# Optimization experiments

Measured on AMD Instinct MI355X. Metric: run time of the kernel, lower is better.

The kernel has to match this reference:

```python
import jax, jax.numpy as jnp
import numpy as np

B, S, E = 8, 1024, 1024
H, DH = 16, 64          # num_head, num_hidden (per-head dim); H*DH == E
DFF, K = 2048, 3        # d_ff hardcoded in EncoderBlock; kernel_size
LN_EPS = 1e-5


def _layer_norm(x):
    # Fresh torch.nn.LayerNorm each call -> gamma=1, beta=0
    mu = jnp.mean(x, axis=-1, keepdims=True)
    var = jnp.mean((x - mu) ** 2, axis=-1, keepdims=True)
    return (x - mu) / jnp.sqrt(var + LN_EPS)


def _causal_conv1d(x, w, b, k):
    # x: [B, C_in, S], w: [C_out, C_in, k] (torch Conv1d layout), left-pad k-1 -> causal
    y = jax.lax.conv_general_dilated(
        x, w, window_strides=(1,), padding=[(k - 1, 0)],
        dimension_numbers=("NCH", "OIH", "NCH"))
    return y + b[None, :, None]


def setup_inputs() -> dict:
    key = jax.random.key(0)
    ks = jax.random.split(key, 14)
    sc = 0.02
    inp = {
        "word": jax.random.normal(ks[0], (B, S, E), jnp.float32),
        # torch Linear weights: [out, in]
        "Wq": jax.random.normal(ks[1], (H * DH, E), jnp.float32) * sc,
        "bq": jnp.zeros((H * DH,), jnp.float32),
        "Wk": jax.random.normal(ks[2], (H * DH, E), jnp.float32) * sc,
        "bk": jnp.zeros((H * DH,), jnp.float32),
        "Wv": jax.random.normal(ks[3], (H * DH, E), jnp.float32) * sc,
        "bv": jnp.zeros((H * DH,), jnp.float32),
        "Wo": jax.random.normal(ks[4], (E, H * DH), jnp.float32) * sc,
        "bo": jnp.zeros((E,), jnp.float32),
        # torch Conv1d weights: [out_ch, in_ch, k]
        "conv1_w": jax.random.normal(ks[5], (DFF, E, K), jnp.float32) * sc,
        "conv1_b": jnp.zeros((DFF,), jnp.float32),
        "conv2_w": jax.random.normal(ks[6], (E, DFF, K), jnp.float32) * sc,
        "conv2_b": jnp.zeros((E,), jnp.float32),
    }
    return inp


def reference(word, Wq, bq, Wk, bk, Wv, bv, Wo, bo, conv1_w, conv1_b, conv2_w, conv2_b):
    # ---- Multi-head self-attention (isMasked=False), dropout = identity (eval) ----
    q = (word @ Wq.T + bq).reshape(B, S, H, DH)   # [B,S,H,DH]
    k = (word @ Wk.T + bk).reshape(B, S, H, DH)
    v = (word @ Wv.T + bv).reshape(B, S, H, DH)
    scores = jnp.einsum("bihd,bjhd->bhij", q, k) / np.sqrt(DH)  # [B,H,S,S]
    attn = jax.nn.softmax(scores, axis=-1)
    outs = jnp.einsum("bhij,bjhd->bihd", attn, v).reshape(B, S, H * DH)
    outs = outs @ Wo.T + bo
    x = _layer_norm(outs + word)                  # residual + LayerNorm

    # ---- Causal conv FFN (k>1 branch) ----
    x_ = jnp.swapaxes(x, -1, -2)                  # [B,E,S]
    h = jax.nn.relu(_causal_conv1d(x_, conv1_w, conv1_b, K))  # [B,DFF,S]
    y = _causal_conv1d(h, conv2_w, conv2_b, K)    # [B,E,S]
    y = jnp.swapaxes(y, -1, -2)                   # [B,S,E]
    out = _layer_norm(y + x)
    return out, attn
```

## Files before the change

kernel.cpp:

```cpp
#include <hip/hip_runtime.h>
#include <stdint.h>

#define B_ 8
#define S_ 1024
#define E_ 1024
#define H_ 16
#define DH_ 64
#define DFF_ 2048
#define KCONV 3

typedef unsigned short u16;
typedef __attribute__((ext_vector_type(8))) short short8;
typedef __attribute__((ext_vector_type(4))) float floatx4;
typedef __attribute__((ext_vector_type(4))) unsigned int uintx4;

__device__ __forceinline__ u16 f2bf(float f) {
  unsigned int u = __builtin_bit_cast(unsigned int, f);
  u += 0x7FFFu + ((u >> 16) & 1u);
  return (u16)(u >> 16);
}
__device__ __forceinline__ float bf2f(u16 x) {
  unsigned int u = ((unsigned int)x) << 16;
  return __builtin_bit_cast(float, u);
}

__device__ __forceinline__ uintx4 ld8_f32_bf(const float* __restrict__ p) {
  floatx4 a = *(const floatx4*)p;
  floatx4 b = *(const floatx4*)(p + 4);
  uintx4 r;
  r.x = (unsigned)f2bf(a[0]) | ((unsigned)f2bf(a[1]) << 16);
  r.y = (unsigned)f2bf(a[2]) | ((unsigned)f2bf(a[3]) << 16);
  r.z = (unsigned)f2bf(b[0]) | ((unsigned)f2bf(b[1]) << 16);
  r.w = (unsigned)f2bf(b[2]) | ((unsigned)f2bf(b[3]) << 16);
  return r;
}

__device__ __forceinline__ void gload16(const void* g, void* l) {
  __builtin_amdgcn_global_load_lds((__attribute__((address_space(1))) void*)g,
                                   (__attribute__((address_space(3))) void*)l,
                                   16, 0, 0);
}

enum { F_BIAS = 1, F_RELU = 2, F_RESID = 4, F_OUTF32 = 8, F_SCALE = 16 };

template <int WR, int WC, int TAPS, int FLAGS, bool AF32, bool WF32>
__global__ void __launch_bounds__(256, 2)
gemm_kernel(const void* __restrict__ A, long aS1, long aS2,
            const void* __restrict__ W, long wS1, long wS2,
            const float* __restrict__ bias, const float* __restrict__ resid,
            void* __restrict__ Cout, long cS1, long cS2,
            int zdiv, int lda, int ldw, int ldc, int Kin, float scale) {
  constexpr bool GL = !AF32 && !WF32;
  constexpr int BM = WR * 64, BN = WC * 64, BK = 64;
  constexpr int LDP = GL ? BK : BK + 8;
  __shared__ __align__(16) u16 As[BM * LDP];
  __shared__ __align__(16) u16 Bs[BN * LDP];

  const int z = blockIdx.z;
  const int zq = z / zdiv, zr = z % zdiv;
  const u16* Ab16 = (const u16*)A + zq * aS1 + zr * aS2;
  const float* Ab32 = (const float*)A + zq * aS1 + zr * aS2;
  const u16* Wb16 = (const u16*)W + zq * wS1 + zr * wS2;
  const float* Wb32 = (const float*)W + zq * wS1 + zr * wS2;
  const long cOff = zq * cS1 + zr * cS2;

  const int m0 = blockIdx.y * BM;
  const int n0 = blockIdx.x * BN;
  const int tid = threadIdx.x;
  const int lane = tid & 63;
  const int wave = tid >> 6;
  const int wrow = wave / WC;
  const int wcol = wave % WC;
  const int lm = lane & 15;
  const int lk = lane >> 4;

  floatx4 acc[4][4];
#pragma unroll
  for (int r = 0; r < 4; ++r)
#pragma unroll
    for (int c = 0; c < 4; ++c) acc[r][c] = floatx4{0.f, 0.f, 0.f, 0.f};

  for (int t = 0; t < TAPS; ++t) {
    for (int k0 = 0; k0 < Kin; k0 += BK) {
      __syncthreads();
      if constexpr (GL) {
#pragma unroll
        for (int it = 0; it < BM * BK / 8 / 256; ++it) {
          int c = tid + it * 256;
          int row = c >> 3;
          int kc = (c & 7) << 3;
          long arow = m0 + row;
          if (TAPS > 1) arow += t - (TAPS - 1);
          gload16(Ab16 + arow * (long)lda + k0 + kc,
                  (char*)As + it * 4096 + wave * 1024);
        }
#pragma unroll
        for (int it = 0; it < BN * BK / 8 / 256; ++it) {
          int c = tid + it * 256;
          int row = c >> 3;
          int kc = (c & 7) << 3;
          long off = (long)(n0 + row) * ldw + (long)t * Kin + k0 + kc;
          gload16(Wb16 + off, (char*)Bs + it * 4096 + wave * 1024);
        }
      } else {
#pragma unroll
        for (int it = 0; it < BM * BK / 8 / 256; ++it) {
          int c = tid + it * 256;
          int row = c >> 3;
          int kc = (c & 7) << 3;
          int grow = m0 + row;
          long arow = grow;
          bool zero = false;
          if (TAPS > 1) {
            int s = grow & (S_ - 1);
            if (s + t - (TAPS - 1) < 0) zero = true;
            arow = (long)grow + t - (TAPS - 1);
          }
          uintx4 val;
          if (zero)
            val = uintx4{0u, 0u, 0u, 0u};
          else if (AF32)
            val = ld8_f32_bf(Ab32 + arow * lda + k0 + kc);
          else
            val = *(const uintx4*)(Ab16 + arow * lda + k0 + kc);
          *(uintx4*)&As[row * LDP + kc] = val;
        }
#pragma unroll
        for (int it = 0; it < BN * BK / 8 / 256; ++it) {
          int c = tid + it * 256;
          int row = c >> 3;
          int kc = (c & 7) << 3;
          long off = (long)(n0 + row) * ldw + (long)t * Kin + k0 + kc;
          uintx4 val;
          if (WF32)
            val = ld8_f32_bf(Wb32 + off);
          else
            val = *(const uintx4*)(Wb16 + off);
          *(uintx4*)&Bs[row * LDP + kc] = val;
        }
      }
      __syncthreads();
      if constexpr (GL && TAPS > 1) {
        if ((m0 & (S_ - 1)) == 0 && t < TAPS - 1) {
          int nz = TAPS - 1 - t;
          if (tid < nz * 8) {
            int row = tid >> 3;
            int kc = (tid & 7) << 3;
            *(uintx4*)&As[row * LDP + kc] = uintx4{0u, 0u, 0u, 0u};
          }
          __syncthreads();
        }
      }
#pragma unroll
      for (int kk = 0; kk < BK; kk += 32) {
        short8 af[4], bfr[4];
#pragma unroll
        for (int r = 0; r < 4; ++r)
          af[r] = *(const short8*)&As[(wrow * 64 + r * 16 + lm) * LDP + kk + lk * 8];
#pragma unroll
        for (int c = 0; c < 4; ++c)
          bfr[c] = *(const short8*)&Bs[(wcol * 64 + c * 16 + lm) * LDP + kk + lk * 8];
#pragma unroll
        for (int r = 0; r < 4; ++r)
#pragma unroll
          for (int c = 0; c < 4; ++c)
            acc[r][c] = __builtin_amdgcn_mfma_f32_16x16x32_bf16(af[r], bfr[c], acc[r][c], 0, 0, 0);
      }
    }
  }

  float* Cf = (float*)Cout;
  u16* Cb = (u16*)Cout;
#pragma unroll
  for (int r = 0; r < 4; ++r) {
#pragma unroll
    for (int c = 0; c < 4; ++c) {
#pragma unroll
      for (int i = 0; i < 4; ++i) {
        int grow = m0 + wrow * 64 + r * 16 + lk * 4 + i;
        int gcol = n0 + wcol * 64 + c * 16 + lm;
        float v = acc[r][c][i];
        if (FLAGS & F_SCALE) v *= scale;
        if (FLAGS & F_BIAS) v += bias[gcol];
        long off = cOff + (long)grow * ldc + gcol;
        if (FLAGS & F_RESID) v += resid[off];
        if (FLAGS & F_RELU) v = v > 0.f ? v : 0.f;
        if (FLAGS & F_OUTF32)
          Cf[off] = v;
        else
          Cb[off] = f2bf(v);
      }
    }
  }
}

__global__ void __launch_bounds__(256)
convert_bf16(const float* __restrict__ in, u16* __restrict__ out, long n) {
  long i = ((long)blockIdx.x * 256 + threadIdx.x) * 8;
  if (i >= n) return;
  *(uintx4*)(out + i) = ld8_f32_bf(in + i);
}

__global__ void __launch_bounds__(256)
softmax_kernel(float* __restrict__ attn) {
  long row = blockIdx.x;
  float* p = attn + row * (long)S_;
  int tid = threadIdx.x;
  float v[4];
  float mx = -3.4e38f;
#pragma unroll
  for (int i = 0; i < 4; ++i) {
    v[i] = p[tid + i * 256];
    mx = fmaxf(mx, v[i]);
  }
#pragma unroll
  for (int o = 32; o > 0; o >>= 1) mx = fmaxf(mx, __shfl_down(mx, o));
  __shared__ float sm[4];
  __shared__ float ss[4];
  if ((tid & 63) == 0) sm[tid >> 6] = mx;
  __syncthreads();
  mx = fmaxf(fmaxf(sm[0], sm[1]), fmaxf(sm[2], sm[3]));
  float s = 0.f;
#pragma unroll
  for (int i = 0; i < 4; ++i) {
    v[i] = __expf(v[i] - mx);
    s += v[i];
  }
#pragma unroll
  for (int o = 32; o > 0; o >>= 1) s += __shfl_down(s, o);
  if ((tid & 63) == 0) ss[tid >> 6] = s;
  __syncthreads();
  s = ss[0] + ss[1] + ss[2] + ss[3];
  float inv = 1.f / s;
#pragma unroll
  for (int i = 0; i < 4; ++i) p[tid + i * 256] = v[i] * inv;
}

template <bool ADD2, bool STOREBF, bool STOREF32>
__global__ void __launch_bounds__(256)
ln_kernel(const float* __restrict__ in1, const float* __restrict__ in2,
          u16* __restrict__ outb, float* __restrict__ outf) {
  long row = blockIdx.x;
  const float* p1 = in1 + row * E_;
  int tid = threadIdx.x;
  float v[4];
  float s = 0.f, s2 = 0.f;
#pragma unroll
  for (int i = 0; i < 4; ++i) {
    float x = p1[tid + i * 256];
    if (ADD2) x += in2[row * E_ + tid + i * 256];
    v[i] = x;
    s += x;
    s2 += x * x;
  }
#pragma unroll
  for (int o = 32; o > 0; o >>= 1) {
    s += __shfl_down(s, o);
    s2 += __shfl_down(s2, o);
  }
  __shared__ float as_[4];
  __shared__ float bs_[4];
  if ((tid & 63) == 0) {
    as_[tid >> 6] = s;
    bs_[tid >> 6] = s2;
  }
  __syncthreads();
  s = as_[0] + as_[1] + as_[2] + as_[3];
  s2 = bs_[0] + bs_[1] + bs_[2] + bs_[3];
  float mean = s * (1.f / E_);
  float var = s2 * (1.f / E_) - mean * mean;
  float rstd = rsqrtf(var + 1e-5f);
#pragma unroll
  for (int i = 0; i < 4; ++i) {
    float y = (v[i] - mean) * rstd;
    if (STOREBF) outb[row * E_ + tid + i * 256] = f2bf(y);
    if (STOREF32) outf[row * E_ + tid + i * 256] = y;
  }
}

__global__ void __launch_bounds__(256)
transpose_v(const u16* __restrict__ v, u16* __restrict__ vT) {
  int bh = blockIdx.y;
  int b = bh / H_, h = bh % H_;
  int s0 = blockIdx.x * 64;
  __shared__ u16 t[64][65];
  int tid = threadIdx.x;
#pragma unroll
  for (int i = 0; i < 16; ++i) {
    int idx = tid + i * 256;
    int r = idx >> 6, c = idx & 63;
    t[r][c] = v[(long)b * S_ * E_ + (long)(s0 + r) * E_ + h * DH_ + c];
  }
  __syncthreads();
#pragma unroll
  for (int i = 0; i < 16; ++i) {
    int idx = tid + i * 256;
    int d = idx >> 6, c = idx & 63;
    vT[((long)bh * DH_ + d) * S_ + s0 + c] = t[c][d];
  }
}

__global__ void __launch_bounds__(256)
transpose_w(const float* __restrict__ w, u16* __restrict__ wt, int F, int Cin) {
  long n = (long)F * Cin * KCONV;
  long i = (long)blockIdx.x * 256 + threadIdx.x;
  if (i >= n) return;
  int e = (int)(i % Cin);
  long tmp = i / Cin;
  int t = (int)(tmp % KCONV);
  int f = (int)(tmp / KCONV);
  wt[i] = f2bf(w[(long)f * Cin * KCONV + (long)e * KCONV + t]);
}

extern "C" void kernel_launch(void* const* d_in, const int* in_sizes, int n_in,
                              void* d_out, int out_size, void* d_ws, size_t ws_size,
                              hipStream_t stream) {
  const float* word = (const float*)d_in[0];
  const float* Wq = (const float*)d_in[1];
  const float* bq = (const float*)d_in[2];
  const float* Wk = (const float*)d_in[3];
  const float* bk = (const float*)d_in[4];
  const float* Wv = (const float*)d_in[5];
  const float* bv = (const float*)d_in[6];
  const float* Wo = (const float*)d_in[7];
  const float* bo = (const float*)d_in[8];
  const float* w1 = (const float*)d_in[9];
  const float* b1 = (const float*)d_in[10];
  const float* w2 = (const float*)d_in[11];
  const float* b2 = (const float*)d_in[12];

  const long MB = 1048576L;
  char* ws = (char*)d_ws;
  u16* q_bf = (u16*)(ws + 0 * MB);
  u16* k_bf = (u16*)(ws + 16 * MB);
  u16* v_bf = (u16*)(ws + 32 * MB);
  u16* vT = (u16*)(ws + 48 * MB);
  u16* outs_bf = (u16*)(ws + 64 * MB);
  u16* w1t = (u16*)(ws + 80 * MB);
  u16* w2t = (u16*)(ws + 92 * MB);
  float* z_f32 = (float*)(ws + 0 * MB);
  u16* x_bf = (u16*)(ws + 32 * MB);
  float* x_f32 = (float*)(ws + 104 * MB);
  u16* h_bf = (u16*)(ws + 136 * MB);
  float* y_f32 = (float*)(ws + 48 * MB);
  u16* word_bf = (u16*)(ws + 104 * MB);
  u16* wq_bf = (u16*)(ws + 136 * MB);
  u16* wk_bf = (u16*)(ws + 138 * MB);
  u16* wv_bf = (u16*)(ws + 140 * MB);
  u16* wo_bf = (u16*)(ws + 142 * MB);

  float* out_f = (float*)d_out;
  float* attn_f = (float*)d_out + (long)B_ * S_ * E_;

  dim3 blk(256);

  {
    long n1 = (long)DFF_ * E_ * KCONV;
    transpose_w<<<dim3((unsigned)((n1 + 255) / 256)), blk, 0, stream>>>(w1, w1t, DFF_, E_);
    long n2 = (long)E_ * DFF_ * KCONV;
    transpose_w<<<dim3((unsigned)((n2 + 255) / 256)), blk, 0, stream>>>(w2, w2t, E_, DFF_);
  }
  {
    long nw = (long)B_ * S_ * E_;
    convert_bf16<<<dim3((unsigned)(nw / 8 / 256)), blk, 0, stream>>>(word, word_bf, nw);
    long nl = (long)E_ * E_;
    unsigned gl = (unsigned)(nl / 8 / 256);
    convert_bf16<<<dim3(gl), blk, 0, stream>>>(Wq, wq_bf, nl);
    convert_bf16<<<dim3(gl), blk, 0, stream>>>(Wk, wk_bf, nl);
    convert_bf16<<<dim3(gl), blk, 0, stream>>>(Wv, wv_bf, nl);
    convert_bf16<<<dim3(gl), blk, 0, stream>>>(Wo, wo_bf, nl);
  }

  dim3 g_sq(E_ / 128, (B_ * S_) / 128, 1);
  gemm_kernel<2, 2, 1, F_BIAS, false, false><<<g_sq, blk, 0, stream>>>(
      word_bf, 0, 0, wq_bf, 0, 0, bq, nullptr, q_bf, 0, 0, 1, E_, E_, E_, E_, 1.f);
  gemm_kernel<2, 2, 1, F_BIAS, false, false><<<g_sq, blk, 0, stream>>>(
      word_bf, 0, 0, wk_bf, 0, 0, bk, nullptr, k_bf, 0, 0, 1, E_, E_, E_, E_, 1.f);
  gemm_kernel<2, 2, 1, F_BIAS, false, false><<<g_sq, blk, 0, stream>>>(
      word_bf, 0, 0, wv_bf, 0, 0, bv, nullptr, v_bf, 0, 0, 1, E_, E_, E_, E_, 1.f);

  dim3 g_sc(S_ / 128, S_ / 128, B_ * H_);
  gemm_kernel<2, 2, 1, F_SCALE | F_OUTF32, false, false><<<g_sc, blk, 0, stream>>>(
      q_bf, (long)S_ * E_, DH_, k_bf, (long)S_ * E_, DH_, nullptr, nullptr,
      attn_f, (long)H_ * S_ * S_, (long)S_ * S_, H_, E_, E_, S_, DH_, 0.125f);

  softmax_kernel<<<dim3(B_ * H_ * S_), blk, 0, stream>>>(attn_f);

  transpose_v<<<dim3(S_ / 64, B_ * H_), blk, 0, stream>>>(v_bf, vT);

  dim3 g_av(1, S_ / 256, B_ * H_);
  gemm_kernel<4, 1, 1, 0, true, false><<<g_av, blk, 0, stream>>>(
      attn_f, (long)H_ * S_ * S_, (long)S_ * S_, vT, (long)H_ * DH_ * S_, (long)DH_ * S_,
      nullptr, nullptr, outs_bf, (long)S_ * E_, DH_, H_, S_, S_, E_, S_, 1.f);

  gemm_kernel<2, 2, 1, F_BIAS | F_RESID | F_OUTF32, false, false><<<g_sq, blk, 0, stream>>>(
      outs_bf, 0, 0, wo_bf, 0, 0, bo, word, z_f32, 0, 0, 1, E_, E_, E_, E_, 1.f);

  ln_kernel<false, true, true><<<dim3(B_ * S_), blk, 0, stream>>>(z_f32, nullptr, x_bf, x_f32);

  dim3 g_c1(DFF_ / 128, (B_ * S_) / 128, 1);
  gemm_kernel<2, 2, 3, F_BIAS | F_RELU, false, false><<<g_c1, blk, 0, stream>>>(
      x_bf, 0, 0, w1t, 0, 0, b1, nullptr, h_bf, 0, 0, 1, E_, KCONV * E_, DFF_, E_, 1.f);

  dim3 g_c2(E_ / 128, (B_ * S_) / 128, 1);
  gemm_kernel<2, 2, 3, F_BIAS | F_OUTF32, false, false><<<g_c2, blk, 0, stream>>>(
      h_bf, 0, 0, w2t, 0, 0, b2, nullptr, y_f32, 0, 0, 1, DFF_, KCONV * DFF_, E_, DFF_, 1.f);

  ln_kernel<true, false, true><<<dim3(B_ * S_), blk, 0, stream>>>(y_f32, x_f32, nullptr, out_f);
}
```

Measured before the change: 1.531 ms.

## Store raw scores in bf16 and recompute softmax inside the PV GEMM load

The QK^T GEMM now writes raw scaled scores as bf16 into a workspace buffer instead of fp32 into the attention output. A finalize kernel computes per-row max and inverse sum, writes the fp32 attn output once, and saves the stats. The PV GEMM then reads the bf16 raw scores and applies exp/normalize on the fly, so it no longer reads the fp32 attn matrix and the in-place fp32 read-modify-write softmax pass goes away. This needs a large workspace and falls back to the old path otherwise; it adds redundant exp work in the GEMM loader, and softmax on bf16-rounded scores may lose accuracy.

```diff
diff --git a/kernel.cpp b/kernel.cpp
--- a/kernel.cpp
+++ b/kernel.cpp
@@ -13,6 +13,7 @@
 typedef __attribute__((ext_vector_type(8))) short short8;
 typedef __attribute__((ext_vector_type(4))) float floatx4;
 typedef __attribute__((ext_vector_type(4))) unsigned int uintx4;
+typedef __attribute__((ext_vector_type(2))) unsigned int uintx2;
 
 __device__ __forceinline__ u16 f2bf(float f) {
   unsigned int u = __builtin_bit_cast(unsigned int, f);
@@ -41,20 +42,31 @@
                                    16, 0, 0);
 }
 
+__device__ __forceinline__ unsigned softpair(unsigned w, float m, float invl) {
+  float a = bf2f((u16)(w & 0xffffu));
+  float b = bf2f((u16)(w >> 16));
+  a = __expf(a - m) * invl;
+  b = __expf(b - m) * invl;
+  return (unsigned)f2bf(a) | ((unsigned)f2bf(b) << 16);
+}
+
 enum { F_BIAS = 1, F_RELU = 2, F_RESID = 4, F_OUTF32 = 8, F_SCALE = 16 };
 
-template <int WR, int WC, int TAPS, int FLAGS, bool AF32, bool WF32>
+template <int WR, int WC, int TAPS, int FLAGS, bool AF32, bool WF32, bool ASOFT>
 __global__ void __launch_bounds__(256, 2)
 gemm_kernel(const void* __restrict__ A, long aS1, long aS2,
             const void* __restrict__ W, long wS1, long wS2,
             const float* __restrict__ bias, const float* __restrict__ resid,
+            const float2* __restrict__ astats,
             void* __restrict__ Cout, long cS1, long cS2,
             int zdiv, int lda, int ldw, int ldc, int Kin, float scale) {
-  constexpr bool GL = !AF32 && !WF32;
+  constexpr bool GLA = !AF32 && !ASOFT;
+  constexpr bool GLB = !WF32;
   constexpr int BM = WR * 64, BN = WC * 64, BK = 64;
-  constexpr int LDP = GL ? BK : BK + 8;
-  __shared__ __align__(16) u16 As[BM * LDP];
-  __shared__ __align__(16) u16 Bs[BN * LDP];
+  constexpr int LDPA = GLA ? BK : BK + 8;
+  constexpr int LDPB = GLB ? BK : BK + 8;
+  __shared__ __align__(16) u16 As[BM * LDPA];
+  __shared__ __align__(16) u16 Bs[BN * LDPB];
 
   const int z = blockIdx.z;
   const int zq = z / zdiv, zr = z % zdiv;
@@ -83,7 +95,7 @@
   for (int t = 0; t < TAPS; ++t) {
     for (int k0 = 0; k0 < Kin; k0 += BK) {
       __syncthreads();
-      if constexpr (GL) {
+      if constexpr (GLA) {
 #pragma unroll
         for (int it = 0; it < BM * BK / 8 / 256; ++it) {
           int c = tid + it * 256;
@@ -93,14 +105,6 @@
           if (TAPS > 1) arow += t - (TAPS - 1);
           gload16(Ab16 + arow * (long)lda + k0 + kc,
                   (char*)As + it * 4096 + wave * 1024);
-        }
-#pragma unroll
-        for (int it = 0; it < BN * BK / 8 / 256; ++it) {
-          int c = tid + it * 256;
-          int row = c >> 3;
-          int kc = (c & 7) << 3;
-          long off = (long)(n0 + row) * ldw + (long)t * Kin + k0 + kc;
-          gload16(Wb16 + off, (char*)Bs + it * 4096 + wave * 1024);
         }
       } else {
 #pragma unroll
@@ -119,12 +123,30 @@
           uintx4 val;
           if (zero)
             val = uintx4{0u, 0u, 0u, 0u};
-          else if (AF32)
+          else if (ASOFT) {
+            uintx4 raw = *(const uintx4*)(Ab16 + arow * lda + k0 + kc);
+            float2 st = astats[(long)z * S_ + grow];
+            val.x = softpair(raw.x, st.x, st.y);
+            val.y = softpair(raw.y, st.x, st.y);
+            val.z = softpair(raw.z, st.x, st.y);
+            val.w = softpair(raw.w, st.x, st.y);
+          } else if (AF32)
             val = ld8_f32_bf(Ab32 + arow * lda + k0 + kc);
           else
             val = *(const uintx4*)(Ab16 + arow * lda + k0 + kc);
-          *(uintx4*)&As[row * LDP + kc] = val;
+          *(uintx4*)&As[row * LDPA + kc] = val;
         }
+      }
+      if constexpr (GLB) {
+#pragma unroll
+        for (int it = 0; it < BN * BK / 8 / 256; ++it) {
+          int c = tid + it * 256;
+          int row = c >> 3;
+          int kc = (c & 7) << 3;
+          long off = (long)(n0 + row) * ldw + (long)t * Kin + k0 + kc;
+          gload16(Wb16 + off, (char*)Bs + it * 4096 + wave * 1024);
+        }
+      } else {
 #pragma unroll
         for (int it = 0; it < BN * BK / 8 / 256; ++it) {
           int c = tid + it * 256;
@@ -136,17 +158,17 @@
             val = ld8_f32_bf(Wb32 + off);
           else
             val = *(const uintx4*)(Wb16 + off);
-          *(uintx4*)&Bs[row * LDP + kc] = val;
+          *(uintx4*)&Bs[row * LDPB + kc] = val;
         }
       }
       __syncthreads();
-      if constexpr (GL && TAPS > 1) {
+      if constexpr (GLA && TAPS > 1) {
         if ((m0 & (S_ - 1)) == 0 && t < TAPS - 1) {
           int nz = TAPS - 1 - t;
           if (tid < nz * 8) {
             int row = tid >> 3;
             int kc = (tid & 7) << 3;
-            *(uintx4*)&As[row * LDP + kc] = uintx4{0u, 0u, 0u, 0u};
+            *(uintx4*)&As[row * LDPA + kc] = uintx4{0u, 0u, 0u, 0u};
           }
           __syncthreads();
         }
@@ -156,10 +178,10 @@
         short8 af[4], bfr[4];
 #pragma unroll
         for (int r = 0; r < 4; ++r)
-          af[r] = *(const short8*)&As[(wrow * 64 + r * 16 + lm) * LDP + kk + lk * 8];
+          af[r] = *(const short8*)&As[(wrow * 64 + r * 16 + lm) * LDPA + kk + lk * 8];
 #pragma unroll
         for (int c = 0; c < 4; ++c)
-          bfr[c] = *(const short8*)&Bs[(wcol * 64 + c * 16 + lm) * LDP + kk + lk * 8];
+          bfr[c] = *(const short8*)&Bs[(wcol * 64 + c * 16 + lm) * LDPB + kk + lk * 8];
 #pragma unroll
         for (int r = 0; r < 4; ++r)
 #pragma unroll
@@ -234,6 +256,45 @@
   float inv = 1.f / s;
 #pragma unroll
   for (int i = 0; i < 4; ++i) p[tid + i * 256] = v[i] * inv;
+}
+
+__global__ void __launch_bounds__(256)
+softmax_finalize(const u16* __restrict__ raw, float* __restrict__ attn,
+                 float2* __restrict__ stats) {
+  long row = blockIdx.x;
+  const u16* p = raw + row * (long)S_;
+  int tid = threadIdx.x;
+  uintx2 w = *(const uintx2*)(p + tid * 4);
+  float v[4];
+  v[0] = bf2f((u16)(w.x & 0xffffu));
+  v[1] = bf2f((u16)(w.x >> 16));
+  v[2] = bf2f((u16)(w.y & 0xffffu));
+  v[3] = bf2f((u16)(w.y >> 16));
+  float mx = fmaxf(fmaxf(v[0], v[1]), fmaxf(v[2], v[3]));
+#pragma unroll
+  for (int o = 32; o > 0; o >>= 1) mx = fmaxf(mx, __shfl_down(mx, o));
+  __shared__ float sm[4];
+  __shared__ float ss[4];
+  if ((tid & 63) == 0) sm[tid >> 6] = mx;
+  __syncthreads();
+  mx = fmaxf(fmaxf(sm[0], sm[1]), fmaxf(sm[2], sm[3]));
+  float s = 0.f;
+#pragma unroll
+  for (int i = 0; i < 4; ++i) {
+    v[i] = __expf(v[i] - mx);
+    s += v[i];
+  }
+#pragma unroll
+  for (int o = 32; o > 0; o >>= 1) s += __shfl_down(s, o);
+  if ((tid & 63) == 0) ss[tid >> 6] = s;
+  __syncthreads();
+  s = ss[0] + ss[1] + ss[2] + ss[3];
+  float inv = 1.f / s;
+  floatx4 outv;
+#pragma unroll
+  for (int i = 0; i < 4; ++i) outv[i] = v[i] * inv;
+  *(floatx4*)(attn + row * (long)S_ + tid * 4) = outv;
+  if (tid == 0) stats[row] = make_float2(mx, inv);
 }
 
 template <bool ADD2, bool STOREBF, bool STOREF32>
@@ -348,6 +409,9 @@
   u16* wk_bf = (u16*)(ws + 138 * MB);
   u16* wv_bf = (u16*)(ws + 140 * MB);
   u16* wo_bf = (u16*)(ws + 142 * MB);
+  u16* raw_bf = (u16*)(ws + 144 * MB);
+  float2* stats = (float2*)(ws + 400 * MB);
+  const bool big_ws = ws_size >= (size_t)(402 * MB);
 
   float* out_f = (float*)d_out;
   float* attn_f = (float*)d_out + (long)B_ * S_ * E_;
@@ -372,39 +436,50 @@
   }
 
   dim3 g_sq(E_ / 128, (B_ * S_) / 128, 1);
-  gemm_kernel<2, 2, 1, F_BIAS, false, false><<<g_sq, blk, 0, stream>>>(
-      word_bf, 0, 0, wq_bf, 0, 0, bq, nullptr, q_bf, 0, 0, 1, E_, E_, E_, E_, 1.f);
-  gemm_kernel<2, 2, 1, F_BIAS, false, false><<<g_sq, blk, 0, stream>>>(
-      word_bf, 0, 0, wk_bf, 0, 0, bk, nullptr, k_bf, 0, 0, 1, E_, E_, E_, E_, 1.f);
-  gemm_kernel<2, 2, 1, F_BIAS, false, false><<<g_sq, blk, 0, stream>>>(
-      word_bf, 0, 0, wv_bf, 0, 0, bv, nullptr, v_bf, 0, 0, 1, E_, E_, E_, E_, 1.f);
+  gemm_kernel<2, 2, 1, F_BIAS, false, false, false><<<g_sq, blk, 0, stream>>>(
+      word_bf, 0, 0, wq_bf, 0, 0, bq, nullptr, nullptr, q_bf, 0, 0, 1, E_, E_, E_, E_, 1.f);
+  gemm_kernel<2, 2, 1, F_BIAS, false, false, false><<<g_sq, blk, 0, stream>>>(
+      word_bf, 0, 0, wk_bf, 0, 0, bk, nullptr, nullptr, k_bf, 0, 0, 1, E_, E_, E_, E_, 1.f);
+  gemm_kernel<2, 2, 1, F_BIAS, false, false, false><<<g_sq, blk, 0, stream>>>(
+      word_bf, 0, 0, wv_bf, 0, 0, bv, nullptr, nullptr, v_bf, 0, 0, 1, E_, E_, E_, E_, 1.f);
 
   dim3 g_sc(S_ / 128, S_ / 128, B_ * H_);
-  gemm_kernel<2, 2, 1, F_SCALE | F_OUTF32, false, false><<<g_sc, blk, 0, stream>>>(
-      q_bf, (long)S_ * E_, DH_, k_bf, (long)S_ * E_, DH_, nullptr, nullptr,
-      attn_f, (long)H_ * S_ * S_, (long)S_ * S_, H_, E_, E_, S_, DH_, 0.125f);
-
-  softmax_kernel<<<dim3(B_ * H_ * S_), blk, 0, stream>>>(attn_f);
+  dim3 g_av(1, S_ / 256, B_ * H_);
 
   transpose_v<<<dim3(S_ / 64, B_ * H_), blk, 0, stream>>>(v_bf, vT);
 
-  dim3 g_av(1, S_ / 256, B_ * H_);
-  gemm_kernel<4, 1, 1, 0, true, false><<<g_av, blk, 0, stream>>>(
-      attn_f, (long)H_ * S_ * S_, (long)S_ * S_, vT, (long)H_ * DH_ * S_, (long)DH_ * S_,
-      nullptr, nullptr, outs_bf, (long)S_ * E_, DH_, H_, S_, S_, E_, S_, 1.f);
-
-  gemm_kernel<2, 2, 1, F_BIAS | F_RESID | F_OUTF32, false, false><<<g_sq, blk, 0, stream>>>(
-      outs_bf, 0, 0, wo_bf, 0, 0, bo, word, z_f32, 0, 0, 1, E_, E_, E_, E_, 1.f);
+  if (big_ws) {
+    gemm_kernel<2, 2, 1, F_SCALE, false, false, false><<<g_sc, blk, 0, stream>>>(
+        q_bf, (long)S_ * E_, DH_, k_bf, (long)S_ * E_, DH_, nullptr, nullptr, nullptr,
+        raw_bf, (long)H_ * S_ * S_, (long)S_ * S_, H_, E_, E_, S_, DH_, 0.125f);
+
+    softmax_finalize<<<dim3(B_ * H_ * S_), blk, 0, stream>>>(raw_bf, attn_f, stats);
+
+    gemm_kernel<4, 1, 1, 0, false, false, true><<<g_av, blk, 0, stream>>>(
+        raw_bf, (long)H_ * S_ * S_, (long)S_ * S_, vT, (long)H_ * DH_ * S_, (long)DH_ * S_,
+        nullptr, nullptr, stats, outs_bf, (long)S_ * E_, DH_, H_, S_, S_, E_, S_, 1.f);
+  } else {
+    gemm_kernel<2, 2, 1, F_SCALE | F_OUTF32, false, false, false><<<g_sc, blk, 0, stream>>>(
+        q_bf, (long)S_ * E_, DH_, k_bf, (long)S_ * E_, DH_, nullptr, nullptr, nullptr,
+        attn_f, (long)H_ * S_ * S_, (long)S_ * S_, H_, E_, E_, S_, DH_, 0.125f);
+    softmax_kernel<<<dim3(B_ * H_ * S_), blk, 0, stream>>>(attn_f);
+    gemm_kernel<4, 1, 1, 0, true, false, false><<<g_av, blk, 0, stream>>>(
+        attn_f, (long)H_ * S_ * S_, (long)S_ * S_, vT, (long)H_ * DH_ * S_, (long)DH_ * S_,
+        nullptr, nullptr, nullptr, outs_bf, (long)S_ * E_, DH_, H_, S_, S_, E_, S_, 1.f);
+  }
+
+  gemm_kernel<2, 2, 1, F_BIAS | F_RESID | F_OUTF32, false, false, false><<<g_sq, blk, 0, stream>>>(
+      outs_bf, 0, 0, wo_bf, 0, 0, bo, word, nullptr, z_f32, 0, 0, 1, E_, E_, E_, E_, 1.f);
 
   ln_kernel<false, true, true><<<dim3(B_ * S_), blk, 0, stream>>>(z_f32, nullptr, x_bf, x_f32);
 
   dim3 g_c1(DFF_ / 128, (B_ * S_) / 128, 1);
-  gemm_kernel<2, 2, 3, F_BIAS | F_RELU, false, false><<<g_c1, blk, 0, stream>>>(
-      x_bf, 0, 0, w1t, 0, 0, b1, nullptr, h_bf, 0, 0, 1, E_, KCONV * E_, DFF_, E_, 1.f);
+  gemm_kernel<2, 2, 3, F_BIAS | F_RELU, false, false, false><<<g_c1, blk, 0, stream>>>(
+      x_bf, 0, 0, w1t, 0, 0, b1, nullptr, nullptr, h_bf, 0, 0, 1, E_, KCONV * E_, DFF_, E_, 1.f);
 
   dim3 g_c2(E_ / 128, (B_ * S_) / 128, 1);
-  gemm_kernel<2, 2, 3, F_BIAS | F_OUTF32, false, false><<<g_c2, blk, 0, stream>>>(
-      h_bf, 0, 0, w2t, 0, 0, b2, nullptr, y_f32, 0, 0, 1, DFF_, KCONV * DFF_, E_, DFF_, 1.f);
+  gemm_kernel<2, 2, 3, F_BIAS | F_OUTF32, false, false, false><<<g_c2, blk, 0, stream>>>(
+      h_bf, 0, 0, w2t, 0, 0, b2, nullptr, nullptr, y_f32, 0, 0, 1, DFF_, KCONV * DFF_, E_, DFF_, 1.f);
 
   ln_kernel<true, false, true><<<dim3(B_ * S_), blk, 0, stream>>>(y_f32, x_f32, nullptr, out_f);
 }
```

Result: faster. 1.410 ms (-7.9%).
